# Kernel tuning notes

Hardware: AMD Instinct MI355X
Metric: run time of the kernel (lower is better)

Reference implementation:

```python
import jax, jax.numpy as jnp
import numpy as np

D = 1024
EPS = 1e-5

def layer_norm(x, g, b):
    m = jnp.mean(x, axis=-1, keepdims=True)
    v = jnp.mean(jnp.square(x - m), axis=-1, keepdims=True)
    return (x - m) * jax.lax.rsqrt(v + EPS) * g + b

def setup_inputs() -> dict:
    key = jax.random.key(0)
    ks = jax.random.split(key, 8)
    S, B = 4096, 4
    s = 1.0 / np.sqrt(D)
    return {
        "x": jax.random.normal(ks[0], (S, B, D), dtype=jnp.float32),
        "W_v": jax.random.uniform(ks[1], (D, D), jnp.float32, -s, s),
        "theta": jax.random.uniform(ks[2], (D, D), jnp.float32, -s, s),
        "ln1_g": jnp.ones((D,), jnp.float32),
        "ln1_b": jnp.zeros((D,), jnp.float32),
        "ln2_g": jnp.ones((D,), jnp.float32),
        "ln2_b": jnp.zeros((D,), jnp.float32),
        "w1": jax.random.uniform(ks[3], (4 * D, D), jnp.float32, -s, s),
        "b1": jnp.zeros((4 * D,), jnp.float32),
        "w2": jax.random.uniform(ks[4], (D, 4 * D), jnp.float32, -1.0 / np.sqrt(4 * D), 1.0 / np.sqrt(4 * D)),
        "b2": jnp.zeros((D,), jnp.float32),
    }

def reference(x, W_v, theta, ln1_g, ln1_b, ln2_g, ln2_b, w1, b1, w2, b2):
    # x: [S, B, D]
    h = layer_norm(x, ln1_g, ln1_b)
    X = jnp.transpose(h, (1, 0, 2))          # [B, n, D], n = S
    n = X.shape[1]
    XWv = X @ W_v.T                          # [B, n, D]
    Xth = X @ theta.T                        # [B, n, D]
    # first term: (1/n) * ones(n,n) @ XWv == seq-mean broadcast over rows
    first = jnp.mean(XWv, axis=1, keepdims=True)
    # second term reassociated: (X @ theta(X)^T) @ XWv == X @ (theta(X)^T @ XWv)
    M = jnp.einsum('bnd,bne->bde', Xth, XWv)  # [B, D, D]
    second = (1.0 / (n * np.sqrt(D))) * jnp.einsum('bnd,bde->bne', X, M)
    attn = first + second                    # [B, n, D]
    X = X + attn
    h = jnp.transpose(X, (1, 0, 2))          # [S, B, D]
    h2 = layer_norm(h, ln2_g, ln2_b)
    mlp = jax.nn.gelu(h2 @ w1.T + b1, approximate=False) @ w2.T + b2
    return h + mlp
```

## Files before the change

kernel.cpp:

```cpp
#include <hip/hip_runtime.h>
#include <math.h>

#define S_ 4096
#define B_ 4
#define D_ 1024
#define R_ (S_*B_)
#define H_ (4*D_)

typedef unsigned short u16;
typedef unsigned int   u32;
typedef __attribute__((ext_vector_type(8))) short bf16x8;
typedef __attribute__((ext_vector_type(4))) float f32x4;

__device__ __forceinline__ u16 f2bf(float f) {
  u32 u = __float_as_uint(f);
  u32 r = (u + 0x7fffu + ((u >> 16) & 1u)) >> 16;
  return (u16)r;
}
__device__ __forceinline__ float bf2f(u16 u) {
  return __uint_as_float(((u32)u) << 16);
}

__device__ __forceinline__ void gl_lds16(const u16* g, u16* l) {
  __builtin_amdgcn_global_load_lds((const __attribute__((address_space(1))) void*)g,
                                   (__attribute__((address_space(3))) void*)l,
                                   16, 0, 0);
}
__device__ __forceinline__ void BAR() {
  asm volatile("s_barrier" ::: "memory");
}

__device__ __forceinline__ float gelu_f(float t) {
  const float u2 = 1.5957691216f * t + 0.0713548162726f * t * t * t;
  return t / (1.0f + __expf(-u2));
}

__global__ __launch_bounds__(256) void f2bf_k(const float* __restrict__ in,
                                              u16* __restrict__ out, int n4) {
  int i = blockIdx.x * 256 + threadIdx.x;
  if (i < n4) {
    float4 v = ((const float4*)in)[i];
    ushort4 o = make_ushort4(f2bf(v.x), f2bf(v.y), f2bf(v.z), f2bf(v.w));
    ((ushort4*)out)[i] = o;
  }
}

template<bool TR>
__global__ __launch_bounds__(256) void ln_k(const float* __restrict__ x,
                                            u16* __restrict__ o,
                                            const float* __restrict__ g,
                                            const float* __restrict__ bb) {
  const int row = blockIdx.x;
  const int tid = threadIdx.x;
  const float4 v = *(const float4*)&x[(long)row * D_ + tid * 4];
  float vv[4] = {v.x, v.y, v.z, v.w};
  float s = vv[0] + vv[1] + vv[2] + vv[3];
  float q = vv[0]*vv[0] + vv[1]*vv[1] + vv[2]*vv[2] + vv[3]*vv[3];
  const int l = tid & 63, w = tid >> 6;
  #pragma unroll
  for (int off = 32; off > 0; off >>= 1) {
    s += __shfl_down(s, off, 64);
    q += __shfl_down(q, off, 64);
  }
  __shared__ float red[8];
  if (l == 0) { red[w] = s; red[4 + w] = q; }
  __syncthreads();
  s = red[0] + red[1] + red[2] + red[3];
  q = red[4] + red[5] + red[6] + red[7];
  const float m   = s * (1.0f / D_);
  const float var = q * (1.0f / D_) - m * m;
  const float inv = rsqrtf(var + 1e-5f);
  const long orow = TR ? ((long)(row % B_) * S_ + (row / B_)) : (long)row;
  const int j = tid * 4;
  ushort4 ou = make_ushort4(
      f2bf((vv[0] - m) * inv * g[j+0] + bb[j+0]),
      f2bf((vv[1] - m) * inv * g[j+1] + bb[j+1]),
      f2bf((vv[2] - m) * inv * g[j+2] + bb[j+2]),
      f2bf((vv[3] - m) * inv * g[j+3] + bb[j+3]));
  *(ushort4*)&o[orow * D_ + j] = ou;
}

__global__ __launch_bounds__(256) void colsum_k(const u16* __restrict__ Xw,
                                                float* __restrict__ first) {
  const int d  = blockIdx.x * 256 + threadIdx.x;
  const int b  = blockIdx.z;
  const int n0 = blockIdx.y * 256;
  const u16* p = Xw + ((long)b * S_ + n0) * D_ + d;
  float s = 0.f;
  #pragma unroll 8
  for (int n = 0; n < 256; ++n) s += bf2f(p[(long)n * D_]);
  atomicAdd(&first[b * D_ + d], s);
}

__global__ __launch_bounds__(256) void tr_k(const u16* __restrict__ in,
                                            u16* __restrict__ out) {
  __shared__ u16 t[64][65];
  const int b  = blockIdx.z;
  const int e0 = blockIdx.x * 64;
  const int n0 = blockIdx.y * 64;
  const int tid = threadIdx.x;
  #pragma unroll
  for (int i = 0; i < 4; ++i) {
    const int v = i * 256 + tid;
    const int r = v >> 4;
    const int c = (v & 15) << 2;
    ushort4 d4 = *(const ushort4*)&in[((long)b * S_ + n0 + r) * D_ + e0 + c];
    t[r][c+0] = d4.x; t[r][c+1] = d4.y; t[r][c+2] = d4.z; t[r][c+3] = d4.w;
  }
  __syncthreads();
  #pragma unroll
  for (int i = 0; i < 4; ++i) {
    const int v = i * 256 + tid;
    const int e = v >> 4;
    const int c = (v & 15) << 2;
    ushort4 o4 = make_ushort4(t[c+0][e], t[c+1][e], t[c+2][e], t[c+3][e]);
    *(ushort4*)&out[((long)b * D_ + e0 + e) * S_ + n0 + c] = o4;
  }
}

template<int EPI>
__global__ __launch_bounds__(256, 2) void gemm_k(
    const u16* __restrict__ A, long sAz,
    const u16* __restrict__ B, long sBz,
    int K, int ldc,
    u16* __restrict__ Cb, long sCz,
    float* __restrict__ Cf,
    const float* __restrict__ vec1,
    float scale)
{
  const int bz = blockIdx.z;
  const u16* Ab = A + (long)bz * sAz;
  const u16* Bb = B + (long)bz * sBz;
  const int row0 = blockIdx.x * 128;
  const int col0 = blockIdx.y * 128;
  const int lda = K;

  __shared__ __align__(16) u16 As[128 * 32];
  __shared__ __align__(16) u16 Bs[128 * 32];

  const int tid = threadIdx.x;
  const int w = tid >> 6;
  const int l = tid & 63;
  const int wr = (w >> 1) * 64;
  const int wc = (w & 1) * 64;

  f32x4 acc[4][4];
  #pragma unroll
  for (int mi = 0; mi < 4; ++mi)
    #pragma unroll
    for (int ni = 0; ni < 4; ++ni) acc[mi][ni] = (f32x4){0.f, 0.f, 0.f, 0.f};

  const int lrow = l & 15;
  const int lo   = l >> 4;

  for (int k0 = 0; k0 < K; k0 += 32) {
    __syncthreads();
    #pragma unroll
    for (int it = 0; it < 2; ++it) {
      const int cb = it * 256 + (w << 6);
      const int c  = cb + l;
      const int r  = c >> 2;
      const int qs = ((c & 3) ^ ((r >> 1) & 3)) << 3;
      gl_lds16(Ab + (long)(row0 + r) * lda + (k0 + qs), &As[cb << 3]);
      gl_lds16(Bb + (long)(col0 + r) * lda + (k0 + qs), &Bs[cb << 3]);
    }
    __syncthreads();

    bf16x8 af[4], bfr[4];
    #pragma unroll
    for (int mi = 0; mi < 4; ++mi) {
      const int R = wr + mi * 16 + lrow;
      af[mi]  = *(const bf16x8*)&As[R * 32 + ((lo ^ ((R >> 1) & 3)) << 3)];
    }
    #pragma unroll
    for (int ni = 0; ni < 4; ++ni) {
      const int R = wc + ni * 16 + lrow;
      bfr[ni] = *(const bf16x8*)&Bs[R * 32 + ((lo ^ ((R >> 1) & 3)) << 3)];
    }
    #pragma unroll
    for (int mi = 0; mi < 4; ++mi)
      #pragma unroll
      for (int ni = 0; ni < 4; ++ni)
        acc[mi][ni] = __builtin_amdgcn_mfma_f32_16x16x32_bf16(af[mi], bfr[ni], acc[mi][ni], 0, 0, 0);
  }

  const int rbase = row0 + wr + (lo << 2);
  const int cbase = col0 + wc + lrow;
  #pragma unroll
  for (int mi = 0; mi < 4; ++mi)
    #pragma unroll
    for (int ni = 0; ni < 4; ++ni)
      #pragma unroll
      for (int r = 0; r < 4; ++r) {
        const int i = rbase + mi * 16 + r;
        const int j = cbase + ni * 16;
        if constexpr (EPI == 0)
          Cb[(long)bz * sCz + (long)i * ldc + j] = f2bf(acc[mi][ni][r]);
      }
  (void)Cf; (void)vec1; (void)scale;
}

template<int EPI>
__global__ __launch_bounds__(512, 2) void gemm256_k(
    const u16* __restrict__ A, long sAz,
    const u16* __restrict__ B, long sBz,
    int K, int ldc,
    u16* __restrict__ Cb, long sCz,
    float* __restrict__ Cf,
    const float* __restrict__ vec1,
    float scale)
{
  const int bz = blockIdx.z;
  const u16* Ab = A + (long)bz * sAz;
  const u16* Bb = B + (long)bz * sBz;
  const int row0 = blockIdx.x * 256;
  const int col0 = blockIdx.y * 256;

  __shared__ __align__(16) u16 Lds[2][2][2][256 * 32];

  const int tid = threadIdx.x;
  const int w   = tid >> 6;
  const int l   = tid & 63;
  const int wm  = w >> 2;
  const int wn  = w & 3;
  const int lr  = l & 15;
  const int lo  = l >> 4;

  const int NKH = K >> 5;
  const int NT  = K >> 6;

  const int rs   = w * 32 + (l >> 2);
  const int qsrc = ((l & 3) ^ ((l >> 3) & 3)) << 3;

  const int qsw = (lo ^ ((lr >> 1) & 3)) << 3;

  auto STAGE = [&](int khg, int op) {
    if (khg >= NKH) return;
    const u16* src = (op ? Bb : Ab) + (long)((op ? col0 : row0) + rs) * K + khg * 32 + qsrc;
    u16* dst = &Lds[(khg >> 1) & 1][khg & 1][op][(w * 2) * 512];
    gl_lds16(src, dst);
    gl_lds16(src + (long)16 * K, dst + 512);
  };

  f32x4 acc[8][4];
  #pragma unroll
  for (int mi = 0; mi < 8; ++mi)
    #pragma unroll
    for (int ni = 0; ni < 4; ++ni) acc[mi][ni] = (f32x4){0.f, 0.f, 0.f, 0.f};

  STAGE(0, 0); STAGE(0, 1);
  STAGE(1, 0); STAGE(1, 1);
  STAGE(2, 0); STAGE(2, 1);
  asm volatile("s_waitcnt vmcnt(8)" ::: "memory");
  BAR();

  for (int kt = 0; kt < NT; ++kt) {
    const u16* L00 = &Lds[kt & 1][0][0][0];
    const u16* L01 = &Lds[kt & 1][0][1][0];
    const u16* L10 = &Lds[kt & 1][1][0][0];
    const u16* L11 = &Lds[kt & 1][1][1][0];
    bf16x8 af[4], bf[4];

    #pragma unroll
    for (int ni = 0; ni < 4; ++ni)
      bf[ni] = *(const bf16x8*)&L01[(wn * 64 + ni * 16 + lr) * 32 + qsw];
    #pragma unroll
    for (int mi = 0; mi < 4; ++mi)
      af[mi] = *(const bf16x8*)&L00[(wm * 128 + mi * 16 + lr) * 32 + qsw];
    STAGE(2 * kt + 3, 0);
    BAR();
    __builtin_amdgcn_s_setprio(1);
    #pragma unroll
    for (int mi = 0; mi < 4; ++mi)
      #pragma unroll
      for (int ni = 0; ni < 4; ++ni)
        acc[mi][ni] = __builtin_amdgcn_mfma_f32_16x16x32_bf16(af[mi], bf[ni], acc[mi][ni], 0, 0, 0);
    __builtin_amdgcn_s_setprio(0);
    BAR();

    #pragma unroll
    for (int mi = 0; mi < 4; ++mi)
      af[mi] = *(const bf16x8*)&L00[(wm * 128 + 64 + mi * 16 + lr) * 32 + qsw];
    STAGE(2 * kt + 3, 1);
    if (kt == NT - 1) asm volatile("s_waitcnt vmcnt(0)" ::: "memory");
    else              asm volatile("s_waitcnt vmcnt(8)" ::: "memory");
    BAR();
    __builtin_amdgcn_s_setprio(1);
    #pragma unroll
    for (int mi = 0; mi < 4; ++mi)
      #pragma unroll
      for (int ni = 0; ni < 4; ++ni)
        acc[4 + mi][ni] = __builtin_amdgcn_mfma_f32_16x16x32_bf16(af[mi], bf[ni], acc[4 + mi][ni], 0, 0, 0);
    __builtin_amdgcn_s_setprio(0);
    BAR();

    #pragma unroll
    for (int ni = 0; ni < 4; ++ni)
      bf[ni] = *(const bf16x8*)&L11[(wn * 64 + ni * 16 + lr) * 32 + qsw];
    #pragma unroll
    for (int mi = 0; mi < 4; ++mi)
      af[mi] = *(const bf16x8*)&L10[(wm * 128 + mi * 16 + lr) * 32 + qsw];
    STAGE(2 * kt + 4, 0);
    BAR();
    __builtin_amdgcn_s_setprio(1);
    #pragma unroll
    for (int mi = 0; mi < 4; ++mi)
      #pragma unroll
      for (int ni = 0; ni < 4; ++ni)
        acc[mi][ni] = __builtin_amdgcn_mfma_f32_16x16x32_bf16(af[mi], bf[ni], acc[mi][ni], 0, 0, 0);
    __builtin_amdgcn_s_setprio(0);
    BAR();

    #pragma unroll
    for (int mi = 0; mi < 4; ++mi)
      af[mi] = *(const bf16x8*)&L10[(wm * 128 + 64 + mi * 16 + lr) * 32 + qsw];
    STAGE(2 * kt + 4, 1);
    if (kt < NT - 2)       asm volatile("s_waitcnt vmcnt(8)" ::: "memory");
    else if (kt == NT - 2) asm volatile("s_waitcnt vmcnt(4)" ::: "memory");
    else                   asm volatile("s_waitcnt vmcnt(0)" ::: "memory");
    BAR();
    __builtin_amdgcn_s_setprio(1);
    #pragma unroll
    for (int mi = 0; mi < 4; ++mi)
      #pragma unroll
      for (int ni = 0; ni < 4; ++ni)
        acc[4 + mi][ni] = __builtin_amdgcn_mfma_f32_16x16x32_bf16(af[mi], bf[ni], acc[4 + mi][ni], 0, 0, 0);
    __builtin_amdgcn_s_setprio(0);
    BAR();
  }

  const int rbase = row0 + wm * 128 + (lo << 2);
  const int cbase = col0 + wn * 64 + lr;
  #pragma unroll
  for (int mi = 0; mi < 8; ++mi) {
    #pragma unroll
    for (int ni = 0; ni < 4; ++ni) {
      #pragma unroll
      for (int r = 0; r < 4; ++r) {
        const int i = rbase + mi * 16 + r;
        const int j = cbase + ni * 16;
        const float a = acc[mi][ni][r];
        if constexpr (EPI == 0) {
          Cb[(long)bz * sCz + (long)i * ldc + j] = f2bf(a);
        } else if constexpr (EPI == 1) {
          const float xv = bf2f(Ab[(long)i * K + j]);
          Cf[((long)i * B_ + bz) * (long)D_ + j] =
              xv + vec1[bz * D_ + j] * (1.0f / S_) + scale * a;
        } else if constexpr (EPI == 2) {
          Cb[(long)i * ldc + j] = f2bf(gelu_f(a + vec1[j]));
        } else {
          const long idx = (long)i * ldc + j;
          Cf[idx] = Cf[idx] + a + vec1[j];
        }
      }
    }
  }
}

extern "C" void kernel_launch(void* const* d_in, const int* in_sizes, int n_in,
                              void* d_out, int out_size, void* d_ws, size_t ws_size,
                              hipStream_t stream) {
  (void)in_sizes; (void)n_in; (void)out_size; (void)ws_size;
  const float* x     = (const float*)d_in[0];
  const float* W_v   = (const float*)d_in[1];
  const float* theta = (const float*)d_in[2];
  const float* ln1g  = (const float*)d_in[3];
  const float* ln1b  = (const float*)d_in[4];
  const float* ln2g  = (const float*)d_in[5];
  const float* ln2b  = (const float*)d_in[6];
  const float* w1    = (const float*)d_in[7];
  const float* b1    = (const float*)d_in[8];
  const float* w2    = (const float*)d_in[9];
  const float* b2    = (const float*)d_in[10];
  float* out = (float*)d_out;

  char* ws = (char*)d_ws;
  const size_t MB = 1024ull * 1024ull;
  u16*   Wv_bf = (u16*)(ws + 0);
  u16*   Th_bf = (u16*)(ws + 2 * MB);
  u16*   w1_bf = (u16*)(ws + 4 * MB);
  u16*   w2_bf = (u16*)(ws + 12 * MB);
  float* first = (float*)(ws + 20 * MB);
  u16*   Mt    = (u16*)(ws + 21 * MB);
  u16*   Xn    = (u16*)(ws + 29 * MB);
  u16*   XWv   = (u16*)(ws + 61 * MB);
  u16*   Xth   = (u16*)(ws + 93 * MB);
  u16*   XWvT  = (u16*)(ws + 125 * MB);
  u16*   XthT  = (u16*)(ws + 157 * MB);
  u16*   h2    = (u16*)(ws + 29 * MB);
  u16*   G     = (u16*)(ws + 61 * MB);

  f2bf_k<<<dim3((D_*D_/4 + 255)/256), 256, 0, stream>>>(W_v,   Wv_bf, D_*D_/4);
  f2bf_k<<<dim3((D_*D_/4 + 255)/256), 256, 0, stream>>>(theta, Th_bf, D_*D_/4);
  f2bf_k<<<dim3((H_*D_/4 + 255)/256), 256, 0, stream>>>(w1,    w1_bf, H_*D_/4);
  f2bf_k<<<dim3((H_*D_/4 + 255)/256), 256, 0, stream>>>(w2,    w2_bf, H_*D_/4);

  ln_k<true><<<dim3(R_), 256, 0, stream>>>(x, Xn, ln1g, ln1b);

  gemm256_k<0><<<dim3(R_/256, D_/256, 2), 512, 0, stream>>>(
      Xn, 0, Wv_bf, (long)D_*D_, D_, D_, XWv, (long)R_*D_, nullptr, nullptr, 0.f);

  hipMemsetAsync(first, 0, B_ * D_ * sizeof(float), stream);
  colsum_k<<<dim3(D_/256, 16, B_), 256, 0, stream>>>(XWv, first);

  tr_k<<<dim3(D_/64, S_/64, B_), 256, 0, stream>>>(XWv, XWvT);
  tr_k<<<dim3(D_/64, S_/64, B_), 256, 0, stream>>>(Xth, XthT);

  gemm_k<0><<<dim3(D_/128, D_/128, B_), 256, 0, stream>>>(
      XWvT, (long)D_*S_, XthT, (long)D_*S_, S_, D_, Mt, (long)D_*D_, nullptr, nullptr, 0.f);

  gemm256_k<1><<<dim3(S_/256, D_/256, B_), 512, 0, stream>>>(
      Xn, (long)S_*D_, Mt, (long)D_*D_, D_, D_, nullptr, 0, out, first,
      1.0f / ((float)S_ * 32.0f));

  ln_k<false><<<dim3(R_), 256, 0, stream>>>(out, h2, ln2g, ln2b);

  gemm256_k<2><<<dim3(R_/256, H_/256, 1), 512, 0, stream>>>(
      h2, 0, w1_bf, 0, D_, H_, G, 0, nullptr, b1, 0.f);
  gemm256_k<3><<<dim3(R_/256, D_/256, 1), 512, 0, stream>>>(
      G, 0, w2_bf, 0, H_, D_, nullptr, 0, out, b2, 0.f);
}
```

Measured before the change: 607.1 us.

## Switch gemm256 to 32x32x16 MFMA with deeper prefetch and block swizzle

Rewrites the 256x256 GEMM inner loop to use 32x32x16 bf16 MFMA tiles with f32x16 accumulators instead of 16x16x32, which halves the fragment loads per FLOP and reduces barrier phases per k-tile from four to two. Prefetch now stages four half-tiles ahead with adjusted vmcnt waits, and block IDs are remapped in groups of 8 to change L2 locality across workgroups. The epilogue is rewritten for the 32x32 output layout, which makes stores less contiguous. The risks are changed LDS bank-conflict behaviour, higher register pressure, and an incorrect wait count or hazard at the LDS buffer boundary.

```diff
diff --git a/kernel.cpp b/kernel.cpp
--- a/kernel.cpp
+++ b/kernel.cpp
@@ -11,6 +11,7 @@
 typedef unsigned int   u32;
 typedef __attribute__((ext_vector_type(8))) short bf16x8;
 typedef __attribute__((ext_vector_type(4))) float f32x4;
+typedef __attribute__((ext_vector_type(16))) float f32x16;
 
 __device__ __forceinline__ u16 f2bf(float f) {
   u32 u = __float_as_uint(f);
@@ -213,8 +214,13 @@
   const int bz = blockIdx.z;
   const u16* Ab = A + (long)bz * sAz;
   const u16* Bb = B + (long)bz * sBz;
-  const int row0 = blockIdx.x * 256;
-  const int col0 = blockIdx.y * 256;
+
+  const int nbx = gridDim.x;
+  const int nxy = nbx * gridDim.y;
+  int bid = blockIdx.y * nbx + blockIdx.x;
+  bid = (bid & 7) * (nxy >> 3) + (bid >> 3);
+  const int row0 = (bid % nbx) * 256;
+  const int col0 = (bid / nbx) * 256;
 
   __shared__ __align__(16) u16 Lds[2][2][2][256 * 32];
 
@@ -223,16 +229,14 @@
   const int l   = tid & 63;
   const int wm  = w >> 2;
   const int wn  = w & 3;
-  const int lr  = l & 15;
-  const int lo  = l >> 4;
+  const int l5  = l & 31;
+  const int hi  = l >> 5;
 
   const int NKH = K >> 5;
   const int NT  = K >> 6;
 
   const int rs   = w * 32 + (l >> 2);
   const int qsrc = ((l & 3) ^ ((l >> 3) & 3)) << 3;
-
-  const int qsw = (lo ^ ((lr >> 1) & 3)) << 3;
 
   auto STAGE = [&](int khg, int op) {
     if (khg >= NKH) return;
@@ -242,46 +246,75 @@
     gl_lds16(src + (long)16 * K, dst + 512);
   };
 
-  f32x4 acc[8][4];
-  #pragma unroll
-  for (int mi = 0; mi < 8; ++mi)
-    #pragma unroll
-    for (int ni = 0; ni < 4; ++ni) acc[mi][ni] = (f32x4){0.f, 0.f, 0.f, 0.f};
-
-  STAGE(0, 0); STAGE(0, 1);
-  STAGE(1, 0); STAGE(1, 1);
-  STAGE(2, 0); STAGE(2, 1);
-  asm volatile("s_waitcnt vmcnt(8)" ::: "memory");
+  const int key = (l5 >> 1) & 3;
+  const int q0  = ((0 + hi) ^ key) << 3;
+  const int q1  = ((2 + hi) ^ key) << 3;
+
+  f32x16 acc[4][2];
+  #pragma unroll
+  for (int mi = 0; mi < 4; ++mi)
+    #pragma unroll
+    for (int ni = 0; ni < 2; ++ni)
+      acc[mi][ni] = (f32x16){0.f,0.f,0.f,0.f, 0.f,0.f,0.f,0.f,
+                             0.f,0.f,0.f,0.f, 0.f,0.f,0.f,0.f};
+
+  STAGE(0, 0); STAGE(0, 1); STAGE(1, 0); STAGE(1, 1);
+  STAGE(2, 0); STAGE(2, 1); STAGE(3, 0); STAGE(3, 1);
+  asm volatile("s_waitcnt vmcnt(12)" ::: "memory");
   BAR();
 
   for (int kt = 0; kt < NT; ++kt) {
-    const u16* L00 = &Lds[kt & 1][0][0][0];
-    const u16* L01 = &Lds[kt & 1][0][1][0];
-    const u16* L10 = &Lds[kt & 1][1][0][0];
-    const u16* L11 = &Lds[kt & 1][1][1][0];
-    bf16x8 af[4], bf[4];
-
-    #pragma unroll
-    for (int ni = 0; ni < 4; ++ni)
-      bf[ni] = *(const bf16x8*)&L01[(wn * 64 + ni * 16 + lr) * 32 + qsw];
-    #pragma unroll
-    for (int mi = 0; mi < 4; ++mi)
-      af[mi] = *(const bf16x8*)&L00[(wm * 128 + mi * 16 + lr) * 32 + qsw];
-    STAGE(2 * kt + 3, 0);
+    const int cur = kt & 1;
+    bf16x8 af[4][2], bf[2][2];
+
+    {
+      const u16* LA = &Lds[cur][0][0][0];
+      const u16* LB = &Lds[cur][0][1][0];
+      #pragma unroll
+      for (int ni = 0; ni < 2; ++ni) {
+        const int R = wn * 64 + ni * 32 + l5;
+        bf[ni][0] = *(const bf16x8*)&LB[R * 32 + q0];
+        bf[ni][1] = *(const bf16x8*)&LB[R * 32 + q1];
+      }
+      #pragma unroll
+      for (int mi = 0; mi < 4; ++mi) {
+        const int R = wm * 128 + mi * 32 + l5;
+        af[mi][0] = *(const bf16x8*)&LA[R * 32 + q0];
+        af[mi][1] = *(const bf16x8*)&LA[R * 32 + q1];
+      }
+    }
+    STAGE(2 * kt + 4, 0); STAGE(2 * kt + 4, 1);
+    if (kt == NT - 1) asm volatile("s_waitcnt vmcnt(4)" ::: "memory");
+    else              asm volatile("s_waitcnt vmcnt(8)" ::: "memory");
     BAR();
     __builtin_amdgcn_s_setprio(1);
     #pragma unroll
     for (int mi = 0; mi < 4; ++mi)
       #pragma unroll
-      for (int ni = 0; ni < 4; ++ni)
-        acc[mi][ni] = __builtin_amdgcn_mfma_f32_16x16x32_bf16(af[mi], bf[ni], acc[mi][ni], 0, 0, 0);
+      for (int ni = 0; ni < 2; ++ni) {
+        acc[mi][ni] = __builtin_amdgcn_mfma_f32_32x32x16_bf16(af[mi][0], bf[ni][0], acc[mi][ni], 0, 0, 0);
+        acc[mi][ni] = __builtin_amdgcn_mfma_f32_32x32x16_bf16(af[mi][1], bf[ni][1], acc[mi][ni], 0, 0, 0);
+      }
     __builtin_amdgcn_s_setprio(0);
     BAR();
 
-    #pragma unroll
-    for (int mi = 0; mi < 4; ++mi)
-      af[mi] = *(const bf16x8*)&L00[(wm * 128 + 64 + mi * 16 + lr) * 32 + qsw];
-    STAGE(2 * kt + 3, 1);
+    {
+      const u16* LA = &Lds[cur][1][0][0];
+      const u16* LB = &Lds[cur][1][1][0];
+      #pragma unroll
+      for (int ni = 0; ni < 2; ++ni) {
+        const int R = wn * 64 + ni * 32 + l5;
+        bf[ni][0] = *(const bf16x8*)&LB[R * 32 + q0];
+        bf[ni][1] = *(const bf16x8*)&LB[R * 32 + q1];
+      }
+      #pragma unroll
+      for (int mi = 0; mi < 4; ++mi) {
+        const int R = wm * 128 + mi * 32 + l5;
+        af[mi][0] = *(const bf16x8*)&LA[R * 32 + q0];
+        af[mi][1] = *(const bf16x8*)&LA[R * 32 + q1];
+      }
+    }
+    STAGE(2 * kt + 5, 0); STAGE(2 * kt + 5, 1);
     if (kt == NT - 1) asm volatile("s_waitcnt vmcnt(0)" ::: "memory");
     else              asm volatile("s_waitcnt vmcnt(8)" ::: "memory");
     BAR();
@@ -289,67 +322,34 @@
     #pragma unroll
     for (int mi = 0; mi < 4; ++mi)
       #pragma unroll
-      for (int ni = 0; ni < 4; ++ni)
-        acc[4 + mi][ni] = __builtin_amdgcn_mfma_f32_16x16x32_bf16(af[mi], bf[ni], acc[4 + mi][ni], 0, 0, 0);
+      for (int ni = 0; ni < 2; ++ni) {
+        acc[mi][ni] = __builtin_amdgcn_mfma_f32_32x32x16_bf16(af[mi][0], bf[ni][0], acc[mi][ni], 0, 0, 0);
+        acc[mi][ni] = __builtin_amdgcn_mfma_f32_32x32x16_bf16(af[mi][1], bf[ni][1], acc[mi][ni], 0, 0, 0);
+      }
     __builtin_amdgcn_s_setprio(0);
     BAR();
-
-    #pragma unroll
-    for (int ni = 0; ni < 4; ++ni)
-      bf[ni] = *(const bf16x8*)&L11[(wn * 64 + ni * 16 + lr) * 32 + qsw];
-    #pragma unroll
-    for (int mi = 0; mi < 4; ++mi)
-      af[mi] = *(const bf16x8*)&L10[(wm * 128 + mi * 16 + lr) * 32 + qsw];
-    STAGE(2 * kt + 4, 0);
-    BAR();
-    __builtin_amdgcn_s_setprio(1);
-    #pragma unroll
-    for (int mi = 0; mi < 4; ++mi)
-      #pragma unroll
-      for (int ni = 0; ni < 4; ++ni)
-        acc[mi][ni] = __builtin_amdgcn_mfma_f32_16x16x32_bf16(af[mi], bf[ni], acc[mi][ni], 0, 0, 0);
-    __builtin_amdgcn_s_setprio(0);
-    BAR();
-
-    #pragma unroll
-    for (int mi = 0; mi < 4; ++mi)
-      af[mi] = *(const bf16x8*)&L10[(wm * 128 + 64 + mi * 16 + lr) * 32 + qsw];
-    STAGE(2 * kt + 4, 1);
-    if (kt < NT - 2)       asm volatile("s_waitcnt vmcnt(8)" ::: "memory");
-    else if (kt == NT - 2) asm volatile("s_waitcnt vmcnt(4)" ::: "memory");
-    else                   asm volatile("s_waitcnt vmcnt(0)" ::: "memory");
-    BAR();
-    __builtin_amdgcn_s_setprio(1);
-    #pragma unroll
-    for (int mi = 0; mi < 4; ++mi)
-      #pragma unroll
-      for (int ni = 0; ni < 4; ++ni)
-        acc[4 + mi][ni] = __builtin_amdgcn_mfma_f32_16x16x32_bf16(af[mi], bf[ni], acc[4 + mi][ni], 0, 0, 0);
-    __builtin_amdgcn_s_setprio(0);
-    BAR();
-  }
-
-  const int rbase = row0 + wm * 128 + (lo << 2);
-  const int cbase = col0 + wn * 64 + lr;
-  #pragma unroll
-  for (int mi = 0; mi < 8; ++mi) {
-    #pragma unroll
-    for (int ni = 0; ni < 4; ++ni) {
-      #pragma unroll
-      for (int r = 0; r < 4; ++r) {
-        const int i = rbase + mi * 16 + r;
-        const int j = cbase + ni * 16;
+  }
+
+  const int jb = col0 + wn * 64 + l5;
+  #pragma unroll
+  for (int mi = 0; mi < 4; ++mi) {
+    #pragma unroll
+    for (int ni = 0; ni < 2; ++ni) {
+      const int j = jb + ni * 32;
+      #pragma unroll
+      for (int r = 0; r < 16; ++r) {
+        const long i = row0 + wm * 128 + mi * 32 + (r & 3) + 8 * (r >> 2) + 4 * hi;
         const float a = acc[mi][ni][r];
         if constexpr (EPI == 0) {
-          Cb[(long)bz * sCz + (long)i * ldc + j] = f2bf(a);
+          Cb[(long)bz * sCz + i * ldc + j] = f2bf(a);
         } else if constexpr (EPI == 1) {
-          const float xv = bf2f(Ab[(long)i * K + j]);
-          Cf[((long)i * B_ + bz) * (long)D_ + j] =
+          const float xv = bf2f(Ab[i * K + j]);
+          Cf[(i * B_ + bz) * (long)D_ + j] =
               xv + vec1[bz * D_ + j] * (1.0f / S_) + scale * a;
         } else if constexpr (EPI == 2) {
-          Cb[(long)i * ldc + j] = f2bf(gelu_f(a + vec1[j]));
+          Cb[i * ldc + j] = f2bf(gelu_f(a + vec1[j]));
         } else {
-          const long idx = (long)i * ldc + j;
+          const long idx = i * ldc + j;
           Cf[idx] = Cf[idx] + a + vec1[j];
         }
       }
```

New measurement: 668.9 us. 1.1x slower.
